# Optimization experiments

Measured on AMD Instinct MI355X. Metric: run time of the kernel, lower is better.

The kernel has to match this reference:

```python
import jax, jax.numpy as jnp
import numpy as np
import math

B, S, H = 2, 2048, 1024
NH, HD = 16, 64
EPS = 1e-12


def setup_inputs() -> dict:
    key = jax.random.key(0)
    ks = jax.random.split(key, 6)
    scale = 1.0 / math.sqrt(H)
    return {
        "hidden_states": jax.random.normal(ks[0], (B, S, H), jnp.float32),
        "Wq": jax.random.normal(ks[1], (H, H), jnp.float32) * scale,
        "bq": jnp.zeros((H,), jnp.float32),
        "Wk": jax.random.normal(ks[2], (H, H), jnp.float32) * scale,
        "bk": jnp.zeros((H,), jnp.float32),
        "Wv": jax.random.normal(ks[3], (H, H), jnp.float32) * scale,
        "bv": jnp.zeros((H,), jnp.float32),
        "Wo": jax.random.normal(ks[4], (H, H), jnp.float32) * scale,
        "bo": jnp.zeros((H,), jnp.float32),
        "gamma": jnp.ones((H,), jnp.float32),
        "beta": jnp.zeros((H,), jnp.float32),
    }


def _heads(x):
    # [B, S, H] -> [B, NH, S, HD]
    return x.reshape(B, S, NH, HD).transpose(0, 2, 1, 3)


def reference(hidden_states, Wq, bq, Wk, bk, Wv, bv, Wo, bo, gamma, beta):
    q = _heads(hidden_states @ Wq + bq)
    k = _heads(hidden_states @ Wk + bk)
    v = _heads(hidden_states @ Wv + bv)
    # scores: [B, NH, S, S]
    scores = jnp.einsum("bhqd,bhkd->bhqk", q, k) / math.sqrt(HD)
    probs = jax.nn.softmax(scores, axis=-1)
    ctx = jnp.einsum("bhqk,bhkd->bhqd", probs, v)
    ctx = ctx.transpose(0, 2, 1, 3).reshape(B, S, H)
    attn_out = ctx @ Wo + bo
    x = attn_out + hidden_states
    mu = jnp.mean(x, axis=-1, keepdims=True)
    var = jnp.var(x, axis=-1, keepdims=True)
    return (x - mu) / jnp.sqrt(var + EPS) * gamma + beta
```

## Files before the change

### kernel.cpp

```cpp
#include <hip/hip_runtime.h>
#include <hip/hip_bf16.h>

#define B_ 2
#define S_ 2048
#define H_ 1024
#define NH_ 16
#define HD_ 64
#define M_ (B_*S_)

typedef __attribute__((ext_vector_type(8))) short bf16x8;
typedef __attribute__((ext_vector_type(4))) short bf16x4;
typedef __attribute__((ext_vector_type(4))) float f32x4;
typedef __attribute__((ext_vector_type(4))) int   i32x4;

__device__ inline float waveReduceSum(float v) {
#pragma unroll
  for (int off = 32; off >= 1; off >>= 1) v += __shfl_xor(v, off);
  return v;
}

__device__ inline short f2bf(float f) {
  union { float f; unsigned u; } v; v.f = f;
  unsigned r = v.u + 0x7fffu + ((v.u >> 16) & 1u);
  return (short)(r >> 16);
}

__device__ inline unsigned cvt_pk_bf16(float lo, float hi) {
  unsigned w;
  asm("v_cvt_pk_bf16_f32 %0, %1, %2" : "=v"(w) : "v"(lo), "v"(hi));
  return w;
}

__device__ inline void async_load16(const void* g, void* l) {
  __builtin_amdgcn_global_load_lds(
      (const __attribute__((address_space(1))) void*)g,
      (__attribute__((address_space(3))) void*)l, 16, 0, 0);
}

__device__ inline int swz8(int r) { return (r & 3) | (((r >> 3) & 1) << 2); }

__global__ __launch_bounds__(256)
void cvt_bf16(const float* __restrict__ in, short* __restrict__ out) {
  const size_t i = (size_t)blockIdx.x * 256 + threadIdx.x;
  float4 v = ((const float4*)in)[i];
  bf16x4 o;
  o[0] = f2bf(v.x); o[1] = f2bf(v.y); o[2] = f2bf(v.z); o[3] = f2bf(v.w);
  ((bf16x4*)out)[i] = o;
}

__global__ __launch_bounds__(256)
void transpose_w4(const float* __restrict__ W0, const float* __restrict__ W1,
                  const float* __restrict__ W2, const float* __restrict__ W3,
                  short* __restrict__ Tqkv, short* __restrict__ To) {
  const float* W; short* T;
  switch (blockIdx.z) {
    case 0: W = W0; T = Tqkv; break;
    case 1: W = W1; T = Tqkv + (size_t)1024 * 1024; break;
    case 2: W = W2; T = Tqkv + (size_t)2048 * 1024; break;
    default: W = W3; T = To; break;
  }
  __shared__ float tile[32][36];
  const int tid = threadIdx.x;
  const int tx = tid & 7, ty = tid >> 3;
  const int k0 = blockIdx.y << 5, n0 = blockIdx.x << 5;
  float4 v = *(const float4*)&W[(size_t)(k0 + ty) * H_ + n0 + (tx << 2)];
  tile[ty][(tx << 2) + 0] = v.x;
  tile[ty][(tx << 2) + 1] = v.y;
  tile[ty][(tx << 2) + 2] = v.z;
  tile[ty][(tx << 2) + 3] = v.w;
  __syncthreads();
  bf16x4 o;
  o[0] = f2bf(tile[(tx << 2) + 0][ty]);
  o[1] = f2bf(tile[(tx << 2) + 1][ty]);
  o[2] = f2bf(tile[(tx << 2) + 2][ty]);
  o[3] = f2bf(tile[(tx << 2) + 3][ty]);
  *(bf16x4*)&T[(size_t)(n0 + ty) * H_ + k0 + (tx << 2)] = o;
}

__global__ __launch_bounds__(256)
void gemm_qkv(const short* __restrict__ A, const short* __restrict__ Bt,
              const float* __restrict__ bq, const float* __restrict__ bk,
              const float* __restrict__ bv, short* __restrict__ Qo,
              short* __restrict__ Ko, short* __restrict__ Vto) {
  __shared__ short A_lds[2][128][32];
  __shared__ short B_lds[2][128][32];
  const int tid = threadIdx.x;
  const int lane = tid & 63, wv = tid >> 6;
  const int l16 = lane & 15, lg = lane >> 4;
  const int wr = wv >> 1, wc = wv & 1;
  const int swzb = (blockIdx.x & 7) * 96 + (blockIdx.x >> 3);
  const int bx = swzb % 24, by = swzb / 24;
  const int m0 = by << 7, n0 = bx << 7;
  const int K = H_;

  const int srow = lane >> 2, soff = (lane & 3) << 3;

  f32x4 acc[4][4] = {};

#pragma unroll
  for (int i = 0; i < 2; ++i) {
    const int c = 2 * wv + i;
    async_load16(A + (size_t)(m0 + 16 * c + srow) * K + soff, &A_lds[0][16 * c][0]);
    async_load16(Bt + (size_t)(n0 + 16 * c + srow) * K + soff, &B_lds[0][16 * c][0]);
  }

  int cur = 0;
  for (int t = 0; t < K / 32; ++t) {
    __syncthreads();
    if (t + 1 < K / 32) {
      const int k0 = (t + 1) << 5;
#pragma unroll
      for (int i = 0; i < 2; ++i) {
        const int c = 2 * wv + i;
        async_load16(A + (size_t)(m0 + 16 * c + srow) * K + k0 + soff,
                     &A_lds[cur ^ 1][16 * c][0]);
        async_load16(Bt + (size_t)(n0 + 16 * c + srow) * K + k0 + soff,
                     &B_lds[cur ^ 1][16 * c][0]);
      }
    }
    bf16x8 af[4], bfr[4];
#pragma unroll
    for (int i = 0; i < 4; ++i)
      af[i] = *(const bf16x8*)&A_lds[cur][64 * wr + 16 * i + l16][8 * lg];
#pragma unroll
    for (int j = 0; j < 4; ++j)
      bfr[j] = *(const bf16x8*)&B_lds[cur][64 * wc + 16 * j + l16][8 * lg];
#pragma unroll
    for (int i = 0; i < 4; ++i)
#pragma unroll
      for (int j = 0; j < 4; ++j)
        acc[i][j] = __builtin_amdgcn_mfma_f32_16x16x32_bf16(af[i], bfr[j], acc[i][j], 0, 0, 0);
    cur ^= 1;
  }

  const int mt = n0 >> 10;
  const float* bias = (mt == 0) ? bq : (mt == 1 ? bk : bv);
  const float qs = (mt == 0) ? 0.125f * 1.4426950408889634f : 1.0f;

  if (mt < 2) {
    short* Out = (mt == 0) ? Qo : Ko;
#pragma unroll
    for (int i = 0; i < 4; ++i) {
#pragma unroll
      for (int j = 0; j < 4; ++j) {
        const int nl = (n0 & 1023) + 64 * wc + 16 * j + l16;
        const float bvl = bias[nl];
        const int h = nl >> 6, d = nl & 63;
#pragma unroll
        for (int r = 0; r < 4; ++r) {
          const int m = m0 + 64 * wr + 16 * i + 4 * lg + r;
          const int b = m >> 11, s = m & (S_ - 1);
          Out[(((size_t)(b * NH_ + h) * S_ + s) << 6) + d] =
              f2bf((acc[i][j][r] + bvl) * qs);
        }
      }
    }
  } else {
#pragma unroll
    for (int i = 0; i < 4; ++i) {
      const int mb = m0 + 64 * wr + 16 * i + 4 * lg;
      const int b = mb >> 11, s = mb & (S_ - 1);
#pragma unroll
      for (int j = 0; j < 4; ++j) {
        const int nl = (n0 & 1023) + 64 * wc + 16 * j + l16;
        const float bvl = bias[nl];
        const int h = nl >> 6, d = nl & 63;
        bf16x4 pk;
#pragma unroll
        for (int r = 0; r < 4; ++r) pk[r] = f2bf(acc[i][j][r] + bvl);
        *(bf16x4*)&Vto[(((size_t)(b * NH_ + h) * HD_ + d) << 11) + s] = pk;
      }
    }
  }
}

__global__ __launch_bounds__(256)
void gemm_o(const short* __restrict__ A, const short* __restrict__ Bt,
            const float* __restrict__ bias, float* __restrict__ C) {
  __shared__ short A_lds[2][128][32];
  __shared__ short B_lds[2][128][32];
  const int tid = threadIdx.x;
  const int lane = tid & 63, wv = tid >> 6;
  const int l16 = lane & 15, lg = lane >> 4;
  const int wr = wv >> 1, wc = wv & 1;
  const int swzb = (blockIdx.x & 7) * 32 + (blockIdx.x >> 3);
  const int bx = swzb & 7, by = swzb >> 3;
  const int m0 = by << 7, n0 = bx << 7;
  const int K = H_;

  const int srow = lane >> 2, soff = (lane & 3) << 3;

  f32x4 acc[4][4] = {};

#pragma unroll
  for (int i = 0; i < 2; ++i) {
    const int c = 2 * wv + i;
    async_load16(A + (size_t)(m0 + 16 * c + srow) * K + soff, &A_lds[0][16 * c][0]);
    async_load16(Bt + (size_t)(n0 + 16 * c + srow) * K + soff, &B_lds[0][16 * c][0]);
  }

  int cur = 0;
  for (int t = 0; t < K / 32; ++t) {
    __syncthreads();
    if (t + 1 < K / 32) {
      const int k0 = (t + 1) << 5;
#pragma unroll
      for (int i = 0; i < 2; ++i) {
        const int c = 2 * wv + i;
        async_load16(A + (size_t)(m0 + 16 * c + srow) * K + k0 + soff,
                     &A_lds[cur ^ 1][16 * c][0]);
        async_load16(Bt + (size_t)(n0 + 16 * c + srow) * K + k0 + soff,
                     &B_lds[cur ^ 1][16 * c][0]);
      }
    }
    bf16x8 af[4], bfr[4];
#pragma unroll
    for (int i = 0; i < 4; ++i)
      af[i] = *(const bf16x8*)&A_lds[cur][64 * wr + 16 * i + l16][8 * lg];
#pragma unroll
    for (int j = 0; j < 4; ++j)
      bfr[j] = *(const bf16x8*)&B_lds[cur][64 * wc + 16 * j + l16][8 * lg];
#pragma unroll
    for (int i = 0; i < 4; ++i)
#pragma unroll
      for (int j = 0; j < 4; ++j)
        acc[i][j] = __builtin_amdgcn_mfma_f32_16x16x32_bf16(af[i], bfr[j], acc[i][j], 0, 0, 0);
    cur ^= 1;
  }

#pragma unroll
  for (int i = 0; i < 4; ++i)
#pragma unroll
    for (int j = 0; j < 4; ++j) {
      const int n = n0 + 64 * wc + 16 * j + l16;
      const float bvl = bias[n];
#pragma unroll
      for (int r = 0; r < 4; ++r) {
        const int m = m0 + 64 * wr + 16 * i + 4 * lg + r;
        C[(size_t)m * H_ + n] = acc[i][j][r] + bvl;
      }
    }
}

#define KVB 64

__global__ __launch_bounds__(256)
void attn_mfma(const short* __restrict__ Qg, const short* __restrict__ Kg,
               const short* __restrict__ Vtg, short* __restrict__ ctxb) {
  __shared__ short K_lds[2][KVB][64];
  __shared__ short V_t[2][KVB][64];

  const int tid  = threadIdx.x;
  const int lane = tid & 63;
  const int wv   = tid >> 6;
  const int l16  = lane & 15, lg = lane >> 4;

  const int swz = (blockIdx.x & 7) * 128 + (blockIdx.x >> 3);
  const int bh = swz >> 5, qb = swz & 31;

  const short* Qh = Qg + ((size_t)bh * S_ << 6);
  const short* Kh = Kg + ((size_t)bh * S_ << 6);
  const short* Vh = Vtg + ((size_t)bh << 6) * S_;

  const int q0 = qb * 64 + wv * 16;

  bf16x8 qf[2];
  qf[0] = *(const bf16x8*)&Qh[((size_t)(q0 + l16) << 6) + 8 * lg];
  qf[1] = *(const bf16x8*)&Qh[((size_t)(q0 + l16) << 6) + 8 * lg + 32];

  const int l16part = ((l16 >> 2) << 3) + (l16 & 3);

  const int srow8 = lane >> 3;
  const int schk  = lane & 7;

  f32x4 o[4] = {};
  float m_run = -1e30f, l_run = 0.f;

#define STAGE(buf, kv0)                                                        \
  {                                                                            \
    _Pragma("unroll")                                                          \
    for (int i_ = 0; i_ < 2; ++i_) {                                           \
      const int row_ = 16 * wv + 8 * i_ + srow8;                               \
      const int ch_ = schk ^ swz8(row_);                                       \
      async_load16(Kh + (((size_t)((kv0) + row_)) << 6) + (ch_ << 3),          \
                   &K_lds[buf][16 * wv + 8 * i_][0]);                          \
      async_load16(Vh + (size_t)row_ * S_ + (kv0) + (ch_ << 3),                \
                   &V_t[buf][16 * wv + 8 * i_][0]);                            \
    }                                                                          \
  }

  STAGE(0, 0)

  int cur = 0;
  for (int t = 0; t < S_ / KVB; ++t) {
    __syncthreads();
    if (t + 1 < S_ / KVB) STAGE(cur ^ 1, (t + 1) * KVB)

    f32x4 s[4] = {};
#pragma unroll
    for (int ks = 0; ks < 2; ++ks)
#pragma unroll
      for (int tt = 0; tt < 4; ++tt) {
        const int krow = ((tt >> 1) << 5) + ((tt & 1) << 2) + l16part;
        const int kch = (lg + 4 * ks) ^ swz8(krow);
        bf16x8 kf = *(const bf16x8*)&K_lds[cur][krow][kch << 3];
        s[tt] = __builtin_amdgcn_mfma_f32_16x16x32_bf16(kf, qf[ks], s[tt], 0, 0, 0);
      }

    float pmax = fmaxf(fmaxf(fmaxf(s[0][0], s[0][1]), fmaxf(s[0][2], s[0][3])),
                       fmaxf(fmaxf(s[1][0], s[1][1]), fmaxf(s[1][2], s[1][3])));
    pmax = fmaxf(pmax,
                 fmaxf(fmaxf(fmaxf(s[2][0], s[2][1]), fmaxf(s[2][2], s[2][3])),
                       fmaxf(fmaxf(s[3][0], s[3][1]), fmaxf(s[3][2], s[3][3]))));
    pmax = fmaxf(pmax, __shfl_xor(pmax, 16));
    pmax = fmaxf(pmax, __shfl_xor(pmax, 32));

    float p[4][4];
    float rs = 0.f;
    if (__any(pmax - m_run > 8.0f)) {
      const float mn = fmaxf(m_run, pmax);
      const float scl = __builtin_amdgcn_exp2f(m_run - mn);
      m_run = mn;
#pragma unroll
      for (int tt = 0; tt < 4; ++tt)
#pragma unroll
        for (int r = 0; r < 4; ++r) {
          p[tt][r] = __builtin_amdgcn_exp2f(s[tt][r] - mn);
          rs += p[tt][r];
        }
      rs += __shfl_xor(rs, 16);
      rs += __shfl_xor(rs, 32);
      l_run = l_run * scl + rs;
      float sclr[4];
#pragma unroll
      for (int r = 0; r < 4; ++r) sclr[r] = __shfl(scl, 4 * lg + r);
#pragma unroll
      for (int tt = 0; tt < 4; ++tt)
#pragma unroll
        for (int r = 0; r < 4; ++r) o[tt][r] *= sclr[r];
    } else {
#pragma unroll
      for (int tt = 0; tt < 4; ++tt)
#pragma unroll
        for (int r = 0; r < 4; ++r) {
          p[tt][r] = __builtin_amdgcn_exp2f(s[tt][r] - m_run);
          rs += p[tt][r];
        }
      rs += __shfl_xor(rs, 16);
      rs += __shfl_xor(rs, 32);
      l_run += rs;
    }

    unsigned w[4][2];
#pragma unroll
    for (int tt = 0; tt < 4; ++tt) {
      w[tt][0] = cvt_pk_bf16(p[tt][0], p[tt][1]);
      w[tt][1] = cvt_pk_bf16(p[tt][2], p[tt][3]);
    }

#pragma unroll
    for (int ks = 0; ks < 2; ++ks) {
      i32x4 aw;
      aw[0] = (int)w[2 * ks][0];
      aw[1] = (int)w[2 * ks][1];
      aw[2] = (int)w[2 * ks + 1][0];
      aw[3] = (int)w[2 * ks + 1][1];
      const bf16x8 pf = __builtin_bit_cast(bf16x8, aw);
#pragma unroll
      for (int tt = 0; tt < 4; ++tt) {
        const int vrow = 16 * tt + l16;
        const int vch = (lg + 4 * ks) ^ swz8(vrow);
        bf16x8 vf = *(const bf16x8*)&V_t[cur][vrow][vch << 3];
        o[tt] = __builtin_amdgcn_mfma_f32_16x16x32_bf16(pf, vf, o[tt], 0, 0, 0);
      }
    }
    cur ^= 1;
  }
#undef STAGE

  float invr[4];
#pragma unroll
  for (int r = 0; r < 4; ++r) invr[r] = 1.f / __shfl(l_run, 4 * lg + r);
  const int b = bh >> 4, h = bh & 15;
#pragma unroll
  for (int r = 0; r < 4; ++r) {
    const int q = q0 + 4 * lg + r;
#pragma unroll
    for (int tt = 0; tt < 4; ++tt)
      ctxb[(((size_t)(b * S_ + q) * NH_ + h) << 6) + 16 * tt + l16] =
          f2bf(o[tt][r] * invr[r]);
  }
}

__global__ __launch_bounds__(256)
void resid_ln(const float* __restrict__ attn_out, const float* __restrict__ hs,
              const float* __restrict__ gamma, const float* __restrict__ beta,
              float* __restrict__ out) {
  __shared__ float reds[4], reds2[4];
  const int row = blockIdx.x;
  const int tid = threadIdx.x;
  const float4* a4 = (const float4*)(attn_out + ((size_t)row << 10));
  const float4* h4 = (const float4*)(hs + ((size_t)row << 10));
  float4 a = a4[tid], h = h4[tid];
  float e0 = a.x + h.x, e1 = a.y + h.y, e2 = a.z + h.z, e3 = a.w + h.w;
  float s  = e0 + e1 + e2 + e3;
  float sq = e0 * e0 + e1 * e1 + e2 * e2 + e3 * e3;
  s = waveReduceSum(s);
  sq = waveReduceSum(sq);
  const int lane = tid & 63, wave = tid >> 6;
  if (lane == 0) { reds[wave] = s; reds2[wave] = sq; }
  __syncthreads();
  const float S1 = reds[0] + reds[1] + reds[2] + reds[3];
  const float S2 = reds2[0] + reds2[1] + reds2[2] + reds2[3];
  const float mu = S1 * (1.f / H_);
  const float var = S2 * (1.f / H_) - mu * mu;
  const float rstd = rsqrtf(var + 1e-12f);
  const float4 g = ((const float4*)gamma)[tid];
  const float4 bb = ((const float4*)beta)[tid];
  float4 o;
  o.x = (e0 - mu) * rstd * g.x + bb.x;
  o.y = (e1 - mu) * rstd * g.y + bb.y;
  o.z = (e2 - mu) * rstd * g.z + bb.z;
  o.w = (e3 - mu) * rstd * g.w + bb.w;
  ((float4*)(out + ((size_t)row << 10)))[tid] = o;
}

extern "C" void kernel_launch(void* const* d_in, const int* in_sizes, int n_in,
                              void* d_out, int out_size, void* d_ws, size_t ws_size,
                              hipStream_t stream) {
  const float* X     = (const float*)d_in[0];
  const float* Wq    = (const float*)d_in[1];
  const float* bq    = (const float*)d_in[2];
  const float* Wk    = (const float*)d_in[3];
  const float* bk    = (const float*)d_in[4];
  const float* Wv    = (const float*)d_in[5];
  const float* bv    = (const float*)d_in[6];
  const float* Wo    = (const float*)d_in[7];
  const float* bo    = (const float*)d_in[8];
  const float* gamma = (const float*)d_in[9];
  const float* beta  = (const float*)d_in[10];
  float* out = (float*)d_out;

  char* ws = (char*)d_ws;
  short* Xbf  = (short*)ws;
  short* Wqkv = (short*)(ws + ( 8u << 20));
  short* Wto  = (short*)(ws + (14u << 20));
  short* Qbf  = (short*)(ws + (16u << 20));
  short* Kbf  = (short*)(ws + (24u << 20));
  short* Vt   = (short*)(ws + (32u << 20));
  short* ctxb = Xbf;
  float* attn = (float*)(ws + (16u << 20));

  dim3 blk(256);
  hipLaunchKernelGGL(cvt_bf16, dim3((M_ * H_) / 1024), blk, 0, stream, X, Xbf);
  hipLaunchKernelGGL(transpose_w4, dim3(32, 32, 4), blk, 0, stream,
                     Wq, Wk, Wv, Wo, Wqkv, Wto);
  hipLaunchKernelGGL(gemm_qkv, dim3(768), blk, 0, stream,
                     Xbf, Wqkv, bq, bk, bv, Qbf, Kbf, Vt);
  hipLaunchKernelGGL(attn_mfma, dim3(1024), blk, 0, stream, Qbf, Kbf, Vt, ctxb);
  hipLaunchKernelGGL(gemm_o, dim3(256), blk, 0, stream, ctxb, Wto, bo, attn);
  hipLaunchKernelGGL(resid_ln, dim3(M_), blk, 0, stream, attn, X, gamma, beta, out);
}
```

Measured before the change: 269.5 us.

## Replace async LDS staging with register-prefetched K/V tiles in flash attention

The attention kernel no longer uses direct global-to-LDS async loads for the next K/V tile. Each thread now loads its next K and V chunks into registers at the top of the iteration and writes them into the other LDS buffer after the MFMA work. This changes how the memory latency overlaps with compute and removes reliance on the async-load path. In exchange it costs extra VGPRs and explicit LDS store instructions, and relies on the existing barrier ordering for double-buffer safety.

```diff
diff --git a/kernel.cpp b/kernel.cpp
--- a/kernel.cpp
+++ b/kernel.cpp
@@ -270,31 +270,35 @@
 
   const int l16part = ((l16 >> 2) << 3) + (l16 & 3);
 
-  const int srow8 = lane >> 3;
-  const int schk  = lane & 7;
+  const int kr = tid >> 2;
+  const int cb = (tid & 3) << 1;
+  const int sz = swz8(kr);
+  const int c1 = ((cb    ) ^ sz) << 3;
+  const int c2 = ((cb + 1) ^ sz) << 3;
 
   f32x4 o[4] = {};
   float m_run = -1e30f, l_run = 0.f;
 
-#define STAGE(buf, kv0)                                                        \
-  {                                                                            \
-    _Pragma("unroll")                                                          \
-    for (int i_ = 0; i_ < 2; ++i_) {                                           \
-      const int row_ = 16 * wv + 8 * i_ + srow8;                               \
-      const int ch_ = schk ^ swz8(row_);                                       \
-      async_load16(Kh + (((size_t)((kv0) + row_)) << 6) + (ch_ << 3),          \
-                   &K_lds[buf][16 * wv + 8 * i_][0]);                          \
-      async_load16(Vh + (size_t)row_ * S_ + (kv0) + (ch_ << 3),                \
-                   &V_t[buf][16 * wv + 8 * i_][0]);                            \
-    }                                                                          \
-  }
-
-  STAGE(0, 0)
+  {
+    *(bf16x8*)&K_lds[0][kr][c1] = *(const bf16x8*)&Kh[((size_t)kr << 6) + (cb << 3)];
+    *(bf16x8*)&K_lds[0][kr][c2] = *(const bf16x8*)&Kh[((size_t)kr << 6) + ((cb + 1) << 3)];
+    *(bf16x8*)&V_t[0][kr][c1]   = *(const bf16x8*)&Vh[(size_t)kr * S_ + (cb << 3)];
+    *(bf16x8*)&V_t[0][kr][c2]   = *(const bf16x8*)&Vh[(size_t)kr * S_ + ((cb + 1) << 3)];
+  }
 
   int cur = 0;
   for (int t = 0; t < S_ / KVB; ++t) {
+    bf16x8 nk0, nk1, nv0, nv1;
+    const bool pre = (t + 1 < S_ / KVB);
+    if (pre) {
+      const size_t kb = (size_t)((t + 1) * KVB + kr) << 6;
+      nk0 = *(const bf16x8*)&Kh[kb + (cb << 3)];
+      nk1 = *(const bf16x8*)&Kh[kb + ((cb + 1) << 3)];
+      const size_t vb = (size_t)kr * S_ + (t + 1) * KVB;
+      nv0 = *(const bf16x8*)&Vh[vb + (cb << 3)];
+      nv1 = *(const bf16x8*)&Vh[vb + ((cb + 1) << 3)];
+    }
     __syncthreads();
-    if (t + 1 < S_ / KVB) STAGE(cur ^ 1, (t + 1) * KVB)
 
     f32x4 s[4] = {};
 #pragma unroll
@@ -374,9 +378,15 @@
         o[tt] = __builtin_amdgcn_mfma_f32_16x16x32_bf16(pf, vf, o[tt], 0, 0, 0);
       }
     }
+
+    if (pre) {
+      *(bf16x8*)&K_lds[cur ^ 1][kr][c1] = nk0;
+      *(bf16x8*)&K_lds[cur ^ 1][kr][c2] = nk1;
+      *(bf16x8*)&V_t[cur ^ 1][kr][c1]   = nv0;
+      *(bf16x8*)&V_t[cur ^ 1][kr][c2]   = nv1;
+    }
     cur ^= 1;
   }
-#undef STAGE
 
   float invr[4];
 #pragma unroll
```

Result: faster. 256.4 us (-4.8%).
